# Performance work log

Hardware: AMD Instinct MI355X
Metric: run time of the kernel (lower is better)

Reference implementation:

```python
import jax, jax.numpy as jnp
import numpy as np

# Model dims
C = 16          # in_channels / d_model
D_INNER = 64    # expand * C, expand = 64 // C = 4
HEADDIM = 4
NHEADS = D_INNER // HEADDIM   # 16
D_STATE = 64
D_CONV = 4
CONV_DIM = D_INNER + 2 * D_STATE        # 192 (x, B, C streams)
D_IN_PROJ = 2 * D_INNER + 2 * D_STATE + NHEADS  # 272 (z, xBC, dt)
# Input volume
BSZ, DD, HH, WW = 8, 32, 16, 16
L = DD * HH * WW  # 8192, multiple of 256 -> exact adaptive max pool
POOL = 256


def setup_inputs():
    key = jax.random.key(0)
    ks = jax.random.split(key, 10)
    x = jax.random.normal(ks[0], (BSZ, C, DD, HH, WW), jnp.float32)
    # 3 independent Mamba2 blocks -> stack params with leading dim 3
    Win = jax.random.normal(ks[1], (3, D_IN_PROJ, C), jnp.float32) / np.sqrt(C).astype(np.float32)
    conv_w = jax.random.normal(ks[2], (3, CONV_DIM, D_CONV), jnp.float32) / np.sqrt(D_CONV).astype(np.float32)
    conv_b = jax.random.normal(ks[3], (3, CONV_DIM), jnp.float32) * 0.1
    dt_bias = jax.random.normal(ks[4], (3, NHEADS), jnp.float32) * 0.5
    A_log = jnp.log(jax.random.uniform(ks[5], (3, NHEADS), jnp.float32, minval=1.0, maxval=16.0))
    Dp = jax.random.normal(ks[6], (3, NHEADS), jnp.float32) * 0.5 + 1.0
    norm_w = jnp.ones((3, D_INNER), jnp.float32)
    Wout = jax.random.normal(ks[7], (3, C, D_INNER), jnp.float32) / np.sqrt(D_INNER).astype(np.float32)
    gamma = jnp.ones((3, C), jnp.float32)
    beta = jnp.zeros((3, C), jnp.float32)
    lin_w = jax.random.normal(ks[8], (3, 1, C), jnp.float32) / np.sqrt(C).astype(np.float32)
    lin_b = jnp.zeros((3, 1), jnp.float32)
    return dict(x=x, Win=Win, conv_w=conv_w, conv_b=conv_b, dt_bias=dt_bias,
                A_log=A_log, Dp=Dp, norm_w=norm_w, Wout=Wout,
                gamma=gamma, beta=beta, lin_w=lin_w, lin_b=lin_b)


def _mamba2(u, Win, conv_w, conv_b, dt_bias, A_log, Dp, norm_w, Wout):
    """Mamba2 block: u (B, L, C) -> (B, L, C). ngroups=1, rmsnorm gated."""
    B, Lx, _ = u.shape
    zxbcdt = jnp.einsum('blc,pc->blp', u, Win)  # (B, L, 272)
    z = zxbcdt[..., :D_INNER]
    xBC = zxbcdt[..., D_INNER:D_INNER + CONV_DIM]
    dt = jax.nn.softplus(zxbcdt[..., D_INNER + CONV_DIM:] + dt_bias)  # (B, L, H)
    # causal depthwise conv over time
    conv = jax.lax.conv_general_dilated(
        jnp.transpose(xBC, (0, 2, 1)), conv_w[:, None, :], (1,),
        [(D_CONV - 1, 0)], feature_group_count=CONV_DIM)
    xBC = jax.nn.silu(jnp.transpose(conv, (0, 2, 1)) + conv_b)
    xh = xBC[..., :D_INNER].reshape(B, Lx, NHEADS, HEADDIM)
    Bm = xBC[..., D_INNER:D_INNER + D_STATE]   # (B, L, N)
    Cm = xBC[..., D_INNER + D_STATE:]          # (B, L, N)
    A = -jnp.exp(A_log)                        # (H,)
    dA = jnp.exp(dt * A)                       # (B, L, H)
    dtx = dt[..., None] * xh                   # (B, L, H, P)

    def step(S, inp):
        dA_t, dtx_t, B_t, C_t = inp
        S = S * dA_t[:, :, None, None] + dtx_t[..., None] * B_t[:, None, None, :]
        y_t = jnp.einsum('bhpn,bn->bhp', S, C_t)
        return S, y_t

    S0 = jnp.zeros((B, NHEADS, HEADDIM, D_STATE), u.dtype)
    xs = (jnp.moveaxis(dA, 1, 0), jnp.moveaxis(dtx, 1, 0),
          jnp.moveaxis(Bm, 1, 0), jnp.moveaxis(Cm, 1, 0))
    _, ys = jax.lax.scan(step, S0, xs)                       # (L, B, H, P)
    y = jnp.moveaxis(ys, 0, 1) + Dp[None, None, :, None] * xh
    y = y.reshape(B, Lx, D_INNER) * jax.nn.silu(z)           # gate first
    y = y * jax.lax.rsqrt(jnp.mean(y * y, -1, keepdims=True) + 1e-5) * norm_w
    return jnp.einsum('bld,cd->blc', y, Wout)


def _proj_pool(y, gamma, beta, lw, lb):
    """ReLU -> BatchNorm1d (batch stats) -> Linear(C,1) -> AdaptiveMaxPool1d(256)."""
    B, Lx, _ = y.shape
    v = jax.nn.relu(y.reshape(-1, C))
    mu = jnp.mean(v, 0)
    var = jnp.mean((v - mu) ** 2, 0)
    v = (v - mu) * jax.lax.rsqrt(var + 1e-5) * gamma + beta
    s = (v @ lw.T + lb).reshape(B, Lx)
    return jnp.max(s.reshape(B, POOL, Lx // POOL), -1)  # (B, 256)


def reference(x, Win, conv_w, conv_b, dt_bias, A_log, Dp, norm_w, Wout,
              gamma, beta, lin_w, lin_b):
    B, Cc, Dd, Hh, Ww = x.shape
    Lx = Dd * Hh * Ww
    fD = jnp.transpose(x.reshape(B, Cc, Lx), (0, 2, 1))
    fH = jnp.transpose(jnp.transpose(x, (0, 1, 3, 4, 2)).reshape(B, Cc, Lx), (0, 2, 1))
    fW = jnp.transpose(jnp.transpose(x, (0, 1, 4, 2, 3)).reshape(B, Cc, Lx), (0, 2, 1))
    seqs = jnp.stack([fD, fH, fW], 0)  # (3, B, L, C)
    ys = jax.vmap(_mamba2)(seqs, Win, conv_w, conv_b, dt_bias, A_log, Dp, norm_w, Wout)
    pooled = jax.vmap(_proj_pool)(ys, gamma, beta, lin_w, lin_b)  # (3, B, 256)
    return jnp.concatenate([pooled[0], pooled[1], pooled[2]], -1)[:, None, :]  # (B,1,768)
```

## Files before the change

kernel.cpp:

```cpp
#include <hip/hip_runtime.h>
#include <math.h>

#define CONVD 192
#define NC 128
#define PW 32
#define LOG2E 1.4426950408889634f
#define LN2f  0.69314718055994531f

#define OFF_DST   0u
#define OFF_CHA   4194304u
#define OFF_YS    4210688u
#define OFF_PART  5259264u
#define PD        5292032u

#define XSW(m, t)   ((m) * 64 + (((((t) >> 2) ^ ((m) & 15)) & 15) << 2) + ((t) & 3))
#define XSW4(m, tq) ((m) * 64 + ((((tq) ^ ((m) & 15)) & 15) << 2))

__device__ __forceinline__ float fast_silu(float x) {
    float e = __builtin_amdgcn_exp2f(-x * LOG2E);
    return x * __builtin_amdgcn_rcpf(1.f + e);
}
__device__ __forceinline__ float fast_softplus(float x) {
    if (x > 20.f) return x;
    float e = __builtin_amdgcn_exp2f(x * LOG2E);
    return LN2f * __builtin_amdgcn_logf(1.f + e);
}

template<int CTRL>
__device__ __forceinline__ float dpp_ror_add(float x) {
    int yi = __builtin_amdgcn_update_dpp(0, __float_as_int(x), CTRL, 0xf, 0xf, false);
    return x + __int_as_float(yi);
}
__device__ __forceinline__ float rowsum16(float x) {
    x = dpp_ror_add<0x128>(x);
    x = dpp_ror_add<0x124>(x);
    x = dpp_ror_add<0x122>(x);
    x = dpp_ror_add<0x121>(x);
    return x;
}

template<int NT>
__device__ __forceinline__ void stage_u(
    const float* __restrict__ x, float* u_s, int b, int l0, int dir, int tid)
{
    for (int i = tid; i < 67 * 16; i += NT) {
        int pos = i >> 4, c = i & 15;
        int l = l0 + pos - 3;
        float v = 0.f;
        if (l >= 0) {
            if (dir == 0) {
                v = x[(b * 16 + c) * 8192 + l];
            } else if (dir == 1) {
                int h = l >> 9, w = (l >> 5) & 15, d = l & 31;
                v = x[(((b * 16 + c) * 32 + d) * 16 + h) * 16 + w];
            } else {
                int w = l >> 9, d = (l >> 4) & 31, h = l & 15;
                v = x[(((b * 16 + c) * 32 + d) * 16 + h) * 16 + w];
            }
        }
        u_s[pos * 17 + c] = v;
    }
}

__global__ __launch_bounds__(512, 6) void k_delta(
    const float* __restrict__ x, const float* __restrict__ Win,
    const float* __restrict__ convw, const float* __restrict__ convb,
    const float* __restrict__ dtb, const float* __restrict__ A_log,
    float* __restrict__ ws, int dir0, int dslm)
{
    __shared__ float u_s[67 * 17];
    __shared__ float xh_c[4096];
    __shared__ float Bs[4096];
    __shared__ float dts[16 * 65];
    __shared__ float wbuf[16 * 65];
    const int tid = threadIdx.x;
    const int ck = blockIdx.x;
    const int b = blockIdx.y;
    const int dir = dir0 + blockIdx.z;
    float* base = ws + (size_t)(dslm * blockIdx.z) * PD;
    float* Dst = base + OFF_DST;
    float* chA = base + OFF_CHA;
    const int l0 = ck * 64;

    stage_u<512>(x, u_s, b, l0, dir, tid);
    __syncthreads();

    const int lane = tid & 63;
    const int wv = __builtin_amdgcn_readfirstlane(tid >> 6);

    float u[16], uh[16];
    {
        const float* ur = &u_s[(lane + 3) * 17];
        #pragma unroll
        for (int k = 0; k < 16; k++) u[k] = ur[k];
        const float* uhr = &u_s[(lane < 3 ? lane : 0) * 17];
        #pragma unroll
        for (int k = 0; k < 16; k++) uh[k] = uhr[k];
    }

    for (int i = 0; i < 18; i++) {
        const int g = wv * 18 + i;
        const int col = (g < 128) ? (64 + g) : (256 + (g - 128));
        const float* wp = Win + (size_t)(dir * 272 + col) * 16;
        float acc = 0.f, hacc = 0.f;
        #pragma unroll
        for (int k = 0; k < 16; k++) {
            acc += u[k] * wp[k];
            hacc += uh[k] * wp[k];
        }
        if (col < 256) {
            const int ch = col - 64;
            float v1 = __shfl_up(acc, 1);
            float v2 = __shfl_up(acc, 2);
            float v3 = __shfl_up(acc, 3);
            float h0 = __shfl(hacc, 0);
            float h1 = __shfl(hacc, 1);
            float h2 = __shfl(hacc, 2);
            float m1 = (lane >= 1) ? v1 : h2;
            float m2 = (lane >= 2) ? v2 : ((lane == 0) ? h1 : h2);
            float m3 = (lane >= 3) ? v3 : ((lane == 0) ? h0 : ((lane == 1) ? h1 : h2));
            const float* cwp = convw + (size_t)(dir * CONVD + ch) * 4;
            float conv = convb[dir * CONVD + ch]
                       + cwp[0] * m3 + cwp[1] * m2 + cwp[2] * m1 + cwp[3] * acc;
            float xv = fast_silu(conv);
            if (ch < 64) xh_c[XSW(ch, lane)] = xv;
            else         Bs[XSW(ch - 64, lane)] = xv;
        } else {
            const int h = col - 256;
            dts[h * 65 + lane] = fast_softplus(acc + dtb[dir * 16 + h]);
        }
    }
    __syncthreads();

    for (int h = wv; h < 16; h += 8) {
        float A2 = -expf(A_log[dir * 16 + h]) * LOG2E;
        float dtv = dts[h * 65 + lane];
        float v = dtv * A2;
        #pragma unroll
        for (int off = 1; off < 64; off <<= 1) {
            float o = __shfl_up(v, off, 64);
            if (lane >= off) v += o;
        }
        float tot = __shfl(v, 63, 64);
        wbuf[h * 65 + lane] = __builtin_amdgcn_exp2f(tot - v) * dtv;
        if (lane == 63) chA[(b * 16 + h) * 128 + ck] = __builtin_amdgcn_exp2f(tot);
    }
    __syncthreads();

    for (int j = tid; j < 4096; j += 512) {
        int hp = j >> 6, t = j & 63;
        xh_c[XSW(hp, t)] *= wbuf[(hp >> 2) * 65 + t];
    }
    __syncthreads();

    if (tid < 256) {
        const int hp4 = tid >> 4, n4 = tid & 15;
        float a[4][4] = {};
        for (int tq = 0; tq < 16; tq++) {
            float4 xv[4], bv[4];
            #pragma unroll
            for (int i2 = 0; i2 < 4; i2++) {
                xv[i2] = *(const float4*)&xh_c[XSW4(4 * hp4 + i2, tq)];
                bv[i2] = *(const float4*)&Bs[XSW4(4 * n4 + i2, tq)];
            }
            #pragma unroll
            for (int i2 = 0; i2 < 4; i2++)
                #pragma unroll
                for (int j2 = 0; j2 < 4; j2++)
                    a[i2][j2] += xv[i2].x * bv[j2].x + xv[i2].y * bv[j2].y
                               + xv[i2].z * bv[j2].z + xv[i2].w * bv[j2].w;
        }
        #pragma unroll
        for (int i2 = 0; i2 < 4; i2++) {
            int hp = 4 * hp4 + i2;
            int h = hp >> 2, p = hp & 3;
            *(float4*)(Dst + ((size_t)((b * 16 + h) * 128 + ck)) * 256 + p * 64 + 4 * n4) =
                make_float4(a[i2][0], a[i2][1], a[i2][2], a[i2][3]);
        }
    }
}

__global__ __launch_bounds__(64) void k_chunk_scan(
    float* __restrict__ ws, int dslm)
{
    float* base = ws + (size_t)(dslm * blockIdx.z) * PD;
    float* Dst = base + OFF_DST;
    const float* chA = base + OFF_CHA;
    const int bh = blockIdx.x >> 2;
    const int elem = (blockIdx.x & 3) * 64 + threadIdx.x;
    float S = 0.f;
    for (int k0 = 0; k0 < NC; k0 += 8) {
        float d[8], av[8];
        #pragma unroll
        for (int j = 0; j < 8; j++) {
            d[j] = Dst[((size_t)(bh * 128 + k0 + j)) * 256 + elem];
            av[j] = chA[bh * 128 + k0 + j];
        }
        #pragma unroll
        for (int j = 0; j < 8; j++) {
            Dst[((size_t)(bh * 128 + k0 + j)) * 256 + elem] = S;
            S = av[j] * S + d[j];
        }
    }
}

__global__ __launch_bounds__(256, 2) void k_out_epi(
    const float* __restrict__ x, const float* __restrict__ Win,
    const float* __restrict__ convw, const float* __restrict__ convb,
    const float* __restrict__ dtb, const float* __restrict__ A_log,
    const float* __restrict__ Dp, const float* __restrict__ normw,
    const float* __restrict__ Wout, float* __restrict__ ws, int dir0, int dslm)
{
    __shared__ float SinT[64 * 68];
    __shared__ float xh_c[4096];
    __shared__ float Bz[4096];
    __shared__ float Cc[4096];
    __shared__ float uW[67 * 17];
    __shared__ float dts[16 * 65];
    __shared__ float ct2l[16 * 65];
    __shared__ float Dps[16];
    __shared__ float red[4][34];
    float* base = ws + (size_t)(dslm * blockIdx.z) * PD;
    const float* Dst = base + OFF_DST;
    float* ys        = base + OFF_YS;
    float* partials  = base + OFF_PART;
    const int dir = dir0 + blockIdx.z;
    const int tid = threadIdx.x;
    const int b = blockIdx.y;
    const int ck = blockIdx.x;
    const int l0 = ck * 64;
    const int t4 = tid >> 4, x4 = tid & 15;
    const int lane = tid & 63;
    const int wv = __builtin_amdgcn_readfirstlane(tid >> 6);

    stage_u<256>(x, uW, b, l0, dir, tid);
    for (int j = tid; j < 1024; j += 256) {
        int hp = j >> 4, n4 = (j & 15) << 2;
        int h = hp >> 2, p = hp & 3;
        float4 sv = *(const float4*)(Dst + ((size_t)((b * 16 + h) * 128 + ck)) * 256 + p * 64 + n4);
        SinT[(n4 + 0) * 68 + hp] = sv.x;
        SinT[(n4 + 1) * 68 + hp] = sv.y;
        SinT[(n4 + 2) * 68 + hp] = sv.z;
        SinT[(n4 + 3) * 68 + hp] = sv.w;
    }
    if (tid < 16) Dps[tid] = Dp[dir * 16 + tid];
    __syncthreads();

    float u[16], uh[16];
    {
        const float* ur = &uW[(lane + 3) * 17];
        #pragma unroll
        for (int k = 0; k < 16; k++) u[k] = ur[k];
        const float* uhr = &uW[(lane < 3 ? lane : 0) * 17];
        #pragma unroll
        for (int k = 0; k < 16; k++) uh[k] = uhr[k];
    }

    for (int i = 0; i < 52; i++) {
        const int col = 64 + wv * 52 + i;
        const float* wp = Win + (size_t)(dir * 272 + col) * 16;
        float acc = 0.f, hacc = 0.f;
        #pragma unroll
        for (int k = 0; k < 16; k++) {
            acc += u[k] * wp[k];
            hacc += uh[k] * wp[k];
        }
        if (col < 256) {
            const int ch = col - 64;
            float v1 = __shfl_up(acc, 1);
            float v2 = __shfl_up(acc, 2);
            float v3 = __shfl_up(acc, 3);
            float h0 = __shfl(hacc, 0);
            float h1 = __shfl(hacc, 1);
            float h2 = __shfl(hacc, 2);
            float m1 = (lane >= 1) ? v1 : h2;
            float m2 = (lane >= 2) ? v2 : ((lane == 0) ? h1 : h2);
            float m3 = (lane >= 3) ? v3 : ((lane == 0) ? h0 : ((lane == 1) ? h1 : h2));
            const float* cwp = convw + (size_t)(dir * CONVD + ch) * 4;
            float conv = convb[dir * CONVD + ch]
                       + cwp[0] * m3 + cwp[1] * m2 + cwp[2] * m1 + cwp[3] * acc;
            float xv = fast_silu(conv);
            if (ch < 64)       xh_c[XSW(ch, lane)] = xv;
            else if (ch < 128) Bz[XSW(ch - 64, lane)] = xv;
            else               Cc[XSW(ch - 128, lane)] = xv;
        } else {
            const int h = col - 256;
            dts[h * 65 + lane] = fast_softplus(acc + dtb[dir * 16 + h]);
        }
    }
    __syncthreads();

    for (int h = wv; h < 16; h += 4) {
        float A2 = -expf(A_log[dir * 16 + h]) * LOG2E;
        float dtv = dts[h * 65 + lane];
        float v = dtv * A2;
        #pragma unroll
        for (int off = 1; off < 64; off <<= 1) {
            float o = __shfl_up(v, off, 64);
            if (lane >= off) v += o;
        }
        ct2l[h * 65 + lane] = v;
    }
    __syncthreads();

    float G_[4][4] = {}, CS_[4][4] = {};
    for (int n = 0; n < 64; n++) {
        float4 cr4 = *(const float4*)&Cc[XSW4(n, t4)];
        float4 br4 = *(const float4*)&Bz[XSW4(n, x4)];
        float cr[4] = {cr4.x, cr4.y, cr4.z, cr4.w};
        float br[4] = {br4.x, br4.y, br4.z, br4.w};
        float sn[4];
        #pragma unroll
        for (int q = 0; q < 4; q++) sn[q] = SinT[n * 68 + 4 * x4 + q];
        #pragma unroll
        for (int r = 0; r < 4; r++)
            #pragma unroll
            for (int q = 0; q < 4; q++) {
                G_[r][q] += cr[r] * br[q];
                CS_[r][q] += cr[r] * sn[q];
            }
    }
    __syncthreads();

    for (int i = 0; i < 16; i++) {
        const int col = wv * 16 + i;
        const float* wp = Win + (size_t)(dir * 272 + col) * 16;
        float acc = 0.f;
        #pragma unroll
        for (int k = 0; k < 16; k++) acc += u[k] * wp[k];
        Bz[XSW(col, lane)] = acc;
    }
    __syncthreads();
    for (int j = tid; j < 1024; j += 256) {
        int c = j >> 6, d = j & 63;
        uW[c * 65 + d] = Wout[dir * 1024 + j] * normw[dir * 64 + d];
    }
    __syncthreads();

    const int tbase = 4 * t4;
    float g[16];
    #pragma unroll 1
    for (int h = 0; h < 16; h++) {
        float ctt[4], ect[4];
        #pragma unroll
        for (int r = 0; r < 4; r++) {
            ctt[r] = ct2l[h * 65 + tbase + r];
            ect[r] = __builtin_amdgcn_exp2f(ctt[r]);
        }
        float acc[4][4] = {};
        #pragma unroll
        for (int q = 0; q < 4; q++) {
            int s = 4 * x4 + q;
            float cs_ = ct2l[h * 65 + s];
            float dtq = dts[h * 65 + s];
            float xv[4];
            #pragma unroll
            for (int p = 0; p < 4; p++) {
                int m = 4 * h + p;
                xv[p] = xh_c[m * 64 + (((x4 ^ (m & 15)) & 15) << 2) + q];
            }
            #pragma unroll
            for (int r = 0; r < 4; r++) {
                float e = __builtin_amdgcn_exp2f(ctt[r] - cs_);
                e = (s <= tbase + r) ? e : 0.f;
                float w = G_[r][q] * e * dtq;
                #pragma unroll
                for (int p = 0; p < 4; p++) acc[r][p] += w * xv[p];
            }
        }
        if (x4 == h) {
            #pragma unroll
            for (int r = 0; r < 4; r++)
                #pragma unroll
                for (int p = 0; p < 4; p++)
                    acc[r][p] += ect[r] * CS_[r][p];
        }
        #pragma unroll
        for (int r = 0; r < 4; r++)
            #pragma unroll
            for (int p = 0; p < 4; p++)
                acc[r][p] = rowsum16(acc[r][p]);
        float outv = acc[0][0];
        #pragma unroll
        for (int r = 0; r < 4; r++)
            #pragma unroll
            for (int p = 0; p < 4; p++)
                if (r || p) outv = (x4 == r * 4 + p) ? acc[r][p] : outv;
        g[h] = outv;
    }

    const int row = tbase + (x4 >> 2);
    const int p = x4 & 3;
    float sumsq = 0.f;
    #pragma unroll
    for (int h = 0; h < 16; h++) {
        int m = 4 * h + p;
        int ax = m * 64 + ((((row >> 2) ^ (m & 15)) & 15) << 2) + (row & 3);
        float xh = xh_c[ax];
        float zv = Bz[ax];
        float val = (g[h] + Dps[h] * xh) * fast_silu(zv);
        g[h] = val;
        sumsq += val * val;
    }
    sumsq += __shfl_xor(sumsq, 1);
    sumsq += __shfl_xor(sumsq, 2);
    float rms = rsqrtf(sumsq * (1.f / 64.f) + 1e-5f);

    float oc[16];
    #pragma unroll
    for (int c = 0; c < 16; c++) {
        float a = 0.f;
        #pragma unroll
        for (int h = 0; h < 16; h++) a += g[h] * uW[c * 65 + 4 * h + p];
        oc[c] = a;
    }
    #pragma unroll
    for (int c = 0; c < 16; c++) {
        oc[c] += __shfl_xor(oc[c], 1);
        oc[c] += __shfl_xor(oc[c], 2);
    }
    float os[4];
    #pragma unroll
    for (int i2 = 0; i2 < 4; i2++) {
        float a0 = (p == 0) ? oc[i2] : oc[4 + i2];
        float a1 = (p == 2) ? oc[8 + i2] : oc[12 + i2];
        os[i2] = (((p & 2) == 0) ? a0 : a1) * rms;
    }
    size_t bl = (size_t)(b * 8192 + l0 + row);
    *(float4*)(ys + bl * 16 + 4 * p) = make_float4(os[0], os[1], os[2], os[3]);

    float bs[4], bq[4];
    #pragma unroll
    for (int i2 = 0; i2 < 4; i2++) {
        float vv = fmaxf(os[i2], 0.f);
        bs[i2] = vv;
        bq[i2] = vv * vv;
    }
    #pragma unroll
    for (int off = 4; off < 64; off <<= 1) {
        #pragma unroll
        for (int i2 = 0; i2 < 4; i2++) {
            bs[i2] += __shfl_xor(bs[i2], off);
            bq[i2] += __shfl_xor(bq[i2], off);
        }
    }
    const int wlane = tid & 63, wvid = tid >> 6;
    if (wlane < 4) {
        #pragma unroll
        for (int i2 = 0; i2 < 4; i2++) {
            red[wvid][4 * wlane + i2] = bs[i2];
            red[wvid][16 + 4 * wlane + i2] = bq[i2];
        }
    }
    __syncthreads();
    if (tid < 32) {
        float a = red[0][tid] + red[1][tid] + red[2][tid] + red[3][tid];
        partials[((size_t)(b * 128 + ck)) * 32 + tid] = a;
    }
}

__global__ __launch_bounds__(256) void k_pool_bn(
    const float* __restrict__ gamma, const float* __restrict__ beta,
    const float* __restrict__ lin_w, const float* __restrict__ lin_b,
    float* __restrict__ ws, float* __restrict__ out, int dir0, int dslm)
{
    float* base = ws + (size_t)(dslm * blockIdx.z) * PD;
    const float* ys = base + OFF_YS;
    const float* partials = base + OFF_PART;
    const int dir = dir0 + blockIdx.z;
    const int tid = threadIdx.x;
    __shared__ float red[8][33];
    __shared__ float cf[18];
    {
        int c = tid & 31, ks = tid >> 5;
        float a = 0.f;
        for (int k = ks * 128; k < ks * 128 + 128; k++) a += partials[k * 32 + c];
        red[ks][c] = a;
    }
    __syncthreads();
    if (tid < 32) {
        float a = 0.f;
        #pragma unroll
        for (int s2 = 1; s2 < 8; s2++) a += red[s2][tid];
        red[0][tid] += a;
    }
    __syncthreads();
    if (tid == 0) {
        float off = lin_b[dir];
        for (int c = 0; c < 16; c++) {
            float mu = red[0][c] * (1.f / 65536.f);
            float var = red[0][16 + c] * (1.f / 65536.f) - mu * mu;
            float inv = rsqrtf(var + 1e-5f);
            float coef = inv * gamma[dir * 16 + c] * lin_w[dir * 16 + c];
            cf[c] = coef;
            off += beta[dir * 16 + c] * lin_w[dir * 16 + c] - mu * coef;
        }
        cf[16] = off;
    }
    __syncthreads();

    const int b = blockIdx.x >> 3;
    const int jg = blockIdx.x & 7;
    const int j = jg * 32 + (tid >> 3);
    const int sub = tid & 7;
    float m = -3.4e38f;
    #pragma unroll
    for (int r = 0; r < 4; r++) {
        int l = j * PW + 8 * r + sub;
        const float* rowp = ys + (size_t)(b * 8192 + l) * 16;
        float sv = cf[16];
        #pragma unroll
        for (int k = 0; k < 4; k++) {
            float4 v4 = *(const float4*)(rowp + 4 * k);
            sv += fmaxf(v4.x, 0.f) * cf[4 * k] + fmaxf(v4.y, 0.f) * cf[4 * k + 1]
                + fmaxf(v4.z, 0.f) * cf[4 * k + 2] + fmaxf(v4.w, 0.f) * cf[4 * k + 3];
        }
        m = fmaxf(m, sv);
    }
    m = fmaxf(m, __shfl_xor(m, 1));
    m = fmaxf(m, __shfl_xor(m, 2));
    m = fmaxf(m, __shfl_xor(m, 4));
    if (sub == 0) out[b * 768 + dir * 256 + j] = m;
}

extern "C" void kernel_launch(void* const* d_in, const int* in_sizes, int n_in,
                              void* d_out, int out_size, void* d_ws, size_t ws_size,
                              hipStream_t stream) {
    const float* x     = (const float*)d_in[0];
    const float* Win   = (const float*)d_in[1];
    const float* convw = (const float*)d_in[2];
    const float* convb = (const float*)d_in[3];
    const float* dtb   = (const float*)d_in[4];
    const float* Alog  = (const float*)d_in[5];
    const float* Dp    = (const float*)d_in[6];
    const float* normw = (const float*)d_in[7];
    const float* Wout  = (const float*)d_in[8];
    const float* gamma = (const float*)d_in[9];
    const float* beta  = (const float*)d_in[10];
    const float* linw  = (const float*)d_in[11];
    const float* linb  = (const float*)d_in[12];
    float* out = (float*)d_out;
    float* ws = (float*)d_ws;

    const bool batched = ws_size >= (size_t)3 * PD * 4;
    const int nz = batched ? 3 : 1;
    const int dslm = batched ? 1 : 0;
    const int nloop = batched ? 1 : 3;

    for (int d0 = 0; d0 < nloop; ++d0) {
        k_delta<<<dim3(128, 8, nz), dim3(512), 0, stream>>>(
            x, Win, convw, convb, dtb, Alog, ws, d0, dslm);
        k_chunk_scan<<<dim3(512, 1, nz), dim3(64), 0, stream>>>(ws, dslm);
        k_out_epi<<<dim3(128, 8, nz), dim3(256), 0, stream>>>(
            x, Win, convw, convb, dtb, Alog, Dp, normw, Wout, ws, d0, dslm);
        k_pool_bn<<<dim3(64, 1, nz), dim3(256), 0, stream>>>(
            gamma, beta, linw, linb, ws, out, d0, dslm);
    }
}
```

Before: 437.9 us.

## Split k_out_epi head loop across two thread groups with 512-thread blocks

Doubles the k_out_epi block to 512 threads and halves each wave's share of the input-projection, conv, z-projection and head loops. The per-head intra-chunk scan is split into two 256-thread groups of eight heads each, with per-head outputs staged in shared memory (reusing the C buffer). The gated RMSNorm, output projection and BN partial sums then run on the first 256 threads only. This aims to raise parallelism and shorten the serial 16-head loop. In exchange it adds an extra barrier, recomputes the G/CS products redundantly in both groups, and the tighter launch bound may force register spills.

Result: faster. 380.8 us (-13.0%).

```diff
diff --git a/kernel.cpp b/kernel.cpp
--- a/kernel.cpp
+++ b/kernel.cpp
@@ -204,17 +204,17 @@
     }
 }
 
-__global__ __launch_bounds__(256, 2) void k_out_epi(
+__global__ __launch_bounds__(512, 4) void k_out_epi(
     const float* __restrict__ x, const float* __restrict__ Win,
     const float* __restrict__ convw, const float* __restrict__ convb,
     const float* __restrict__ dtb, const float* __restrict__ A_log,
     const float* __restrict__ Dp, const float* __restrict__ normw,
     const float* __restrict__ Wout, float* __restrict__ ws, int dir0, int dslm)
 {
-    __shared__ float SinT[64 * 68];
+    __shared__ float SinT[64 * 65];
     __shared__ float xh_c[4096];
     __shared__ float Bz[4096];
-    __shared__ float Cc[4096];
+    __shared__ float Cy[4352];
     __shared__ float uW[67 * 17];
     __shared__ float dts[16 * 65];
     __shared__ float ct2l[16 * 65];
@@ -229,19 +229,21 @@
     const int b = blockIdx.y;
     const int ck = blockIdx.x;
     const int l0 = ck * 64;
-    const int t4 = tid >> 4, x4 = tid & 15;
+    const int tg = tid & 255;
+    const int t4 = tg >> 4, x4 = tg & 15;
+    const int grp = tid >> 8;
     const int lane = tid & 63;
     const int wv = __builtin_amdgcn_readfirstlane(tid >> 6);
 
-    stage_u<256>(x, uW, b, l0, dir, tid);
-    for (int j = tid; j < 1024; j += 256) {
+    stage_u<512>(x, uW, b, l0, dir, tid);
+    for (int j = tid; j < 1024; j += 512) {
         int hp = j >> 4, n4 = (j & 15) << 2;
         int h = hp >> 2, p = hp & 3;
         float4 sv = *(const float4*)(Dst + ((size_t)((b * 16 + h) * 128 + ck)) * 256 + p * 64 + n4);
-        SinT[(n4 + 0) * 68 + hp] = sv.x;
-        SinT[(n4 + 1) * 68 + hp] = sv.y;
-        SinT[(n4 + 2) * 68 + hp] = sv.z;
-        SinT[(n4 + 3) * 68 + hp] = sv.w;
+        SinT[(n4 + 0) * 65 + hp] = sv.x;
+        SinT[(n4 + 1) * 65 + hp] = sv.y;
+        SinT[(n4 + 2) * 65 + hp] = sv.z;
+        SinT[(n4 + 3) * 65 + hp] = sv.w;
     }
     if (tid < 16) Dps[tid] = Dp[dir * 16 + tid];
     __syncthreads();
@@ -256,8 +258,8 @@
         for (int k = 0; k < 16; k++) uh[k] = uhr[k];
     }
 
-    for (int i = 0; i < 52; i++) {
-        const int col = 64 + wv * 52 + i;
+    for (int i = 0; i < 26; i++) {
+        const int col = 64 + wv * 26 + i;
         const float* wp = Win + (size_t)(dir * 272 + col) * 16;
         float acc = 0.f, hacc = 0.f;
         #pragma unroll
@@ -282,7 +284,7 @@
             float xv = fast_silu(conv);
             if (ch < 64)       xh_c[XSW(ch, lane)] = xv;
             else if (ch < 128) Bz[XSW(ch - 64, lane)] = xv;
-            else               Cc[XSW(ch - 128, lane)] = xv;
+            else               Cy[XSW(ch - 128, lane)] = xv;
         } else {
             const int h = col - 256;
             dts[h * 65 + lane] = fast_softplus(acc + dtb[dir * 16 + h]);
@@ -290,7 +292,7 @@
     }
     __syncthreads();
 
-    for (int h = wv; h < 16; h += 4) {
+    for (int h = wv; h < 16; h += 8) {
         float A2 = -expf(A_log[dir * 16 + h]) * LOG2E;
         float dtv = dts[h * 65 + lane];
         float v = dtv * A2;
@@ -305,13 +307,13 @@
 
     float G_[4][4] = {}, CS_[4][4] = {};
     for (int n = 0; n < 64; n++) {
-        float4 cr4 = *(const float4*)&Cc[XSW4(n, t4)];
+        float4 cr4 = *(const float4*)&Cy[XSW4(n, t4)];
         float4 br4 = *(const float4*)&Bz[XSW4(n, x4)];
         float cr[4] = {cr4.x, cr4.y, cr4.z, cr4.w};
         float br[4] = {br4.x, br4.y, br4.z, br4.w};
         float sn[4];
         #pragma unroll
-        for (int q = 0; q < 4; q++) sn[q] = SinT[n * 68 + 4 * x4 + q];
+        for (int q = 0; q < 4; q++) sn[q] = SinT[n * 65 + 4 * x4 + q];
         #pragma unroll
         for (int r = 0; r < 4; r++)
             #pragma unroll
@@ -322,8 +324,8 @@
     }
     __syncthreads();
 
-    for (int i = 0; i < 16; i++) {
-        const int col = wv * 16 + i;
+    for (int i = 0; i < 8; i++) {
+        const int col = wv * 8 + i;
         const float* wp = Win + (size_t)(dir * 272 + col) * 16;
         float acc = 0.f;
         #pragma unroll
@@ -331,16 +333,17 @@
         Bz[XSW(col, lane)] = acc;
     }
     __syncthreads();
-    for (int j = tid; j < 1024; j += 256) {
+    for (int j = tid; j < 1024; j += 512) {
         int c = j >> 6, d = j & 63;
         uW[c * 65 + d] = Wout[dir * 1024 + j] * normw[dir * 64 + d];
     }
     __syncthreads();
 
+    float* yv = Cy;
     const int tbase = 4 * t4;
-    float g[16];
     #pragma unroll 1
-    for (int h = 0; h < 16; h++) {
+    for (int hh = 0; hh < 8; hh++) {
+        const int h = 8 * grp + hh;
         float ctt[4], ect[4];
         #pragma unroll
         for (int r = 0; r < 4; r++) {
@@ -386,70 +389,76 @@
             #pragma unroll
             for (int p = 0; p < 4; p++)
                 if (r || p) outv = (x4 == r * 4 + p) ? acc[r][p] : outv;
-        g[h] = outv;
-    }
-
-    const int row = tbase + (x4 >> 2);
-    const int p = x4 & 3;
-    float sumsq = 0.f;
-    #pragma unroll
-    for (int h = 0; h < 16; h++) {
-        int m = 4 * h + p;
-        int ax = m * 64 + ((((row >> 2) ^ (m & 15)) & 15) << 2) + (row & 3);
-        float xh = xh_c[ax];
-        float zv = Bz[ax];
-        float val = (g[h] + Dps[h] * xh) * fast_silu(zv);
-        g[h] = val;
-        sumsq += val * val;
-    }
-    sumsq += __shfl_xor(sumsq, 1);
-    sumsq += __shfl_xor(sumsq, 2);
-    float rms = rsqrtf(sumsq * (1.f / 64.f) + 1e-5f);
-
-    float oc[16];
-    #pragma unroll
-    for (int c = 0; c < 16; c++) {
-        float a = 0.f;
-        #pragma unroll
-        for (int h = 0; h < 16; h++) a += g[h] * uW[c * 65 + 4 * h + p];
-        oc[c] = a;
-    }
-    #pragma unroll
-    for (int c = 0; c < 16; c++) {
-        oc[c] += __shfl_xor(oc[c], 1);
-        oc[c] += __shfl_xor(oc[c], 2);
-    }
+        const int row = tbase + (x4 >> 2);
+        const int pp = x4 & 3;
+        yv[(row * 4 + pp) * 17 + h] = outv;
+    }
+    __syncthreads();
+
     float os[4];
-    #pragma unroll
-    for (int i2 = 0; i2 < 4; i2++) {
-        float a0 = (p == 0) ? oc[i2] : oc[4 + i2];
-        float a1 = (p == 2) ? oc[8 + i2] : oc[12 + i2];
-        os[i2] = (((p & 2) == 0) ? a0 : a1) * rms;
-    }
-    size_t bl = (size_t)(b * 8192 + l0 + row);
-    *(float4*)(ys + bl * 16 + 4 * p) = make_float4(os[0], os[1], os[2], os[3]);
-
-    float bs[4], bq[4];
-    #pragma unroll
-    for (int i2 = 0; i2 < 4; i2++) {
-        float vv = fmaxf(os[i2], 0.f);
-        bs[i2] = vv;
-        bq[i2] = vv * vv;
-    }
-    #pragma unroll
-    for (int off = 4; off < 64; off <<= 1) {
+    const int row = tid >> 2;
+    const int p = tid & 3;
+    if (tid < 256) {
+        float gg[16], sumsq = 0.f;
+        #pragma unroll
+        for (int h = 0; h < 16; h++) {
+            float yval = yv[(row * 4 + p) * 17 + h];
+            int m = 4 * h + p;
+            int ax = m * 64 + ((((row >> 2) ^ (m & 15)) & 15) << 2) + (row & 3);
+            float xh = xh_c[ax];
+            float zv = Bz[ax];
+            float val = (yval + Dps[h] * xh) * fast_silu(zv);
+            gg[h] = val;
+            sumsq += val * val;
+        }
+        sumsq += __shfl_xor(sumsq, 1);
+        sumsq += __shfl_xor(sumsq, 2);
+        float rms = rsqrtf(sumsq * (1.f / 64.f) + 1e-5f);
+
+        float oc[16];
+        #pragma unroll
+        for (int c = 0; c < 16; c++) {
+            float a = 0.f;
+            #pragma unroll
+            for (int h = 0; h < 16; h++) a += gg[h] * uW[c * 65 + 4 * h + p];
+            oc[c] = a;
+        }
+        #pragma unroll
+        for (int c = 0; c < 16; c++) {
+            oc[c] += __shfl_xor(oc[c], 1);
+            oc[c] += __shfl_xor(oc[c], 2);
+        }
         #pragma unroll
         for (int i2 = 0; i2 < 4; i2++) {
-            bs[i2] += __shfl_xor(bs[i2], off);
-            bq[i2] += __shfl_xor(bq[i2], off);
-        }
-    }
-    const int wlane = tid & 63, wvid = tid >> 6;
-    if (wlane < 4) {
+            float a0 = (p == 0) ? oc[i2] : oc[4 + i2];
+            float a1 = (p == 2) ? oc[8 + i2] : oc[12 + i2];
+            os[i2] = (((p & 2) == 0) ? a0 : a1) * rms;
+        }
+        size_t bl = (size_t)(b * 8192 + l0 + row);
+        *(float4*)(ys + bl * 16 + 4 * p) = make_float4(os[0], os[1], os[2], os[3]);
+
+        float bs[4], bq[4];
         #pragma unroll
         for (int i2 = 0; i2 < 4; i2++) {
-            red[wvid][4 * wlane + i2] = bs[i2];
-            red[wvid][16 + 4 * wlane + i2] = bq[i2];
+            float vv = fmaxf(os[i2], 0.f);
+            bs[i2] = vv;
+            bq[i2] = vv * vv;
+        }
+        #pragma unroll
+        for (int off = 4; off < 64; off <<= 1) {
+            #pragma unroll
+            for (int i2 = 0; i2 < 4; i2++) {
+                bs[i2] += __shfl_xor(bs[i2], off);
+                bq[i2] += __shfl_xor(bq[i2], off);
+            }
+        }
+        const int wlane = tid & 63, wvid = tid >> 6;
+        if (wlane < 4) {
+            #pragma unroll
+            for (int i2 = 0; i2 < 4; i2++) {
+                red[wvid][4 * wlane + i2] = bs[i2];
+                red[wvid][16 + 4 * wlane + i2] = bq[i2];
+            }
         }
     }
     __syncthreads();
@@ -551,7 +560,7 @@
         k_delta<<<dim3(128, 8, nz), dim3(512), 0, stream>>>(
             x, Win, convw, convb, dtb, Alog, ws, d0, dslm);
         k_chunk_scan<<<dim3(512, 1, nz), dim3(64), 0, stream>>>(ws, dslm);
-        k_out_epi<<<dim3(128, 8, nz), dim3(256), 0, stream>>>(
+        k_out_epi<<<dim3(128, 8, nz), dim3(512), 0, stream>>>(
             x, Win, convw, convb, dtb, Alog, Dp, normw, Wout, ws, d0, dslm);
         k_pool_bn<<<dim3(64, 1, nz), dim3(256), 0, stream>>>(
             gamma, beta, linw, linb, ws, out, d0, dslm);
```
